# Optimization experiments

Measured on AMD Instinct MI355X. Metric: run time of the kernel, lower is better.

The kernel has to match this reference:

```python
import jax, jax.numpy as jnp
import numpy as np

B, S, D, H, L, V, FFM = 4, 2048, 512, 8, 6, 8000, 4
HD = D // H
FF = FFM * D


def setup_inputs() -> dict:
    key = jax.random.key(0)
    ks = jax.random.split(key, 12)
    sc = 0.02
    return {
        "tokens": jax.random.randint(ks[0], (B, S), 0, V),
        "embed": jax.random.normal(ks[1], (V, D), jnp.float32) * sc,
        "wq": jax.random.normal(ks[2], (L, D, D), jnp.float32) * sc,
        "wk": jax.random.normal(ks[3], (L, D, D), jnp.float32) * sc,
        "wv": jax.random.normal(ks[4], (L, D, D), jnp.float32) * sc,
        "wo": jax.random.normal(ks[5], (L, D, D), jnp.float32) * sc,
        "bo": jnp.zeros((L, D), jnp.float32),
        "w1": jax.random.normal(ks[6], (L, D, FF), jnp.float32) * sc,
        "b1": jnp.zeros((L, FF), jnp.float32),
        "w2": jax.random.normal(ks[7], (L, FF, D), jnp.float32) * sc,
        "b2": jnp.zeros((L, D), jnp.float32),
        "ln_g": jnp.ones((L, D), jnp.float32),
        "ln_b": jnp.zeros((L, D), jnp.float32),
        "lnf_g": jnp.ones((D,), jnp.float32),
        "lnf_b": jnp.zeros((D,), jnp.float32),
        "w_out": jax.random.normal(ks[8], (D, V), jnp.float32) * sc,
        "b_out": jnp.zeros((V,), jnp.float32),
    }


def _layernorm(x, g, b, eps=1e-5):
    m = jnp.mean(x, -1, keepdims=True)
    v = jnp.var(x, -1, keepdims=True)
    return (x - m) * jax.lax.rsqrt(v + eps) * g + b


def _pos_encoding():
    pos = jnp.arange(S, dtype=jnp.float32)[:, None]
    div = jnp.exp(jnp.arange(0, D, 2, dtype=jnp.float32) * (-np.log(10000.0) / D))
    pe = jnp.zeros((S, D), jnp.float32)
    pe = pe.at[:, 0::2].set(jnp.sin(pos * div))
    pe = pe.at[:, 1::2].set(jnp.cos(pos * div))
    return pe


def _forward(tokens, embed, wq, wk, wv, wo, bo, w1, b1, w2, b2, ln_g, ln_b,
             lnf_g, lnf_b, w_out, b_out):
    x = embed[tokens] + _pos_encoding()[None]  # [B,S,D]
    causal = jnp.tril(jnp.ones((S, S), bool))
    neg_inf = jnp.float32(-jnp.inf)
    # NOTE: original scales scores by 1/sqrt(n_embd) (key.weight.size(-1) == D)
    inv_scale = 1.0 / jnp.sqrt(jnp.float32(D))

    def block(x, p):
        pwq, pwk, pwv, pwo, pbo, pw1, pb1, pw2, pb2, g, b = p
        # attention sublayer (same LayerNorm params used for both sublayers,
        # matching the repo's reuse of add_and_norm_1)
        h = _layernorm(x, g, b)
        q = (h @ pwq).reshape(B, S, H, HD)
        k = (h @ pwk).reshape(B, S, H, HD)
        v = (h @ pwv).reshape(B, S, H, HD)
        scores = jnp.einsum('bqhd,bkhd->bhqk', q, k) * inv_scale
        scores = jnp.where(causal, scores, neg_inf)
        att = jax.nn.softmax(scores, axis=-1)
        o = jnp.einsum('bhqk,bkhd->bqhd', att, v).reshape(B, S, D)
        x = x + o @ pwo + pbo
        # FFN sublayer
        h2 = _layernorm(x, g, b)
        x = x + jax.nn.relu(h2 @ pw1 + pb1) @ pw2 + pb2
        return x, None

    params = (wq, wk, wv, wo, bo, w1, b1, w2, b2, ln_g, ln_b)
    x, _ = jax.lax.scan(block, x, params)
    x = _layernorm(x, lnf_g, lnf_b)
    logits = x @ w_out + b_out  # [B,S,V]
    return logits


def reference(tokens, embed, wq, wk, wv, wo, bo, w1, b1, w2, b2, ln_g, ln_b,
              lnf_g, lnf_b, w_out, b_out):
    return _forward(tokens, embed, wq, wk, wv, wo, bo, w1, b1, w2, b2,
                    ln_g, ln_b, lnf_g, lnf_b, w_out, b_out)
```

## Files before the change

### kernel.cpp

```cpp
#include <hip/hip_runtime.h>

#define Bsz 4
#define Ssz 2048
#define Dsz 512
#define Hsz 8
#define Lsz 6
#define Vsz 8000
#define FFsz 2048
#define Msz (Bsz*Ssz)
#define VszPad 8192

typedef unsigned short u16;
typedef unsigned int u32;
typedef __attribute__((ext_vector_type(8))) short bf16x8;
typedef __attribute__((ext_vector_type(4))) float f32x4;
typedef __attribute__((ext_vector_type(16))) float f32x16;
typedef __attribute__((ext_vector_type(4))) u32 u32x4;

__device__ __forceinline__ u16 f2b(float f) {
    union { float f; unsigned u; } x; x.f = f;
    return (u16)((x.u + 0x7fffu + ((x.u >> 16) & 1u)) >> 16);
}
__device__ __forceinline__ float b2f(u16 v) {
    union { u32 u; float f; } x; x.u = ((u32)v) << 16; return x.f;
}

#define GLOAD_LDS16(g, l) __builtin_amdgcn_global_load_lds( \
    (const __attribute__((address_space(1))) u32*)(g), \
    (__attribute__((address_space(3))) u32*)(l), 16, 0, 0)

__global__ __launch_bounds__(256) void embed_kernel(const int* __restrict__ tokens,
                                                    const float* __restrict__ embed,
                                                    u16* __restrict__ x) {
    int idx = blockIdx.x * 256 + threadIdx.x;
    int row = idx >> 8, p = idx & 255;
    int tok = tokens[row];
    int s = row & (Ssz - 1);
    float div = __expf((float)p * (-9.210340371976184f / 256.f));
    float ang = (float)s * div;
    float2 e = ((const float2*)(embed + (size_t)tok * Dsz))[p];
    u32 o = (u32)f2b(e.x + sinf(ang)) | ((u32)f2b(e.y + cosf(ang)) << 16);
    ((u32*)(x + (size_t)row * Dsz))[p] = o;
}

__global__ __launch_bounds__(256) void ln_kernel(const u16* __restrict__ x,
                                                 const float* __restrict__ g,
                                                 const float* __restrict__ bta,
                                                 u16* __restrict__ out) {
    int wave = threadIdx.x >> 6, lane = threadIdx.x & 63;
    int row = blockIdx.x * 4 + wave;
    bf16x8 a = ((const bf16x8*)(x + (size_t)row * Dsz))[lane];
    float vals[8];
    #pragma unroll
    for (int i = 0; i < 8; ++i) vals[i] = b2f((u16)a[i]);
    float s = 0.f;
    #pragma unroll
    for (int i = 0; i < 8; ++i) s += vals[i];
    #pragma unroll
    for (int o = 32; o; o >>= 1) s += __shfl_xor(s, o);
    float mean = s * (1.f / 512.f);
    float sq = 0.f;
    #pragma unroll
    for (int i = 0; i < 8; ++i) { float d = vals[i] - mean; sq += d * d; }
    #pragma unroll
    for (int o = 32; o; o >>= 1) sq += __shfl_xor(sq, o);
    float rstd = rsqrtf(sq * (1.f / 512.f) + 1e-5f);
    int base = lane * 8;
    bf16x8 rv;
    #pragma unroll
    for (int i = 0; i < 8; ++i)
        rv[i] = (short)f2b((vals[i] - mean) * rstd * g[base + i] + bta[base + i]);
    *(bf16x8*)(out + (size_t)row * Dsz + base) = rv;
}

__global__ __launch_bounds__(256) void tconv_kernel(const float* __restrict__ src,
                                                    u16* __restrict__ dst,
                                                    int R, int C,
                                                    size_t sstride, size_t dstride) {
    __shared__ float tile[32][33];
    const float* s = src + blockIdx.z * sstride;
    u16* d = dst + blockIdx.z * dstride;
    int c0 = blockIdx.x * 32, r0 = blockIdx.y * 32;
    int tx = threadIdx.x & 31, ty = threadIdx.x >> 5;
    #pragma unroll
    for (int i = 0; i < 32; i += 8)
        tile[ty + i][tx] = s[(size_t)(r0 + ty + i) * C + c0 + tx];
    __syncthreads();
    #pragma unroll
    for (int i = 0; i < 32; i += 8)
        d[(size_t)(c0 + ty + i) * R + r0 + tx] = f2b(tile[tx][ty + i]);
}

__global__ __launch_bounds__(256) void vtrans_kernel(const u16* __restrict__ qkv,
                                                     u16* __restrict__ vT) {
    __shared__ u16 tile[32][33];
    int bh = blockIdx.z, b = bh >> 3, hh = bh & 7;
    int s0 = blockIdx.x * 32, d0 = blockIdx.y * 32;
    int tx = threadIdx.x & 31, ty = threadIdx.x >> 5;
    #pragma unroll
    for (int i = 0; i < 32; i += 8)
        tile[ty + i][tx] = qkv[(size_t)(b * Ssz + s0 + ty + i) * 1536 + 1024 + hh * 64 + d0 + tx];
    __syncthreads();
    #pragma unroll
    for (int i = 0; i < 32; i += 8)
        vT[((size_t)bh * 64 + d0 + ty + i) * Ssz + s0 + tx] = tile[tx][ty + i];
}

template<bool BIAS, bool RES, bool RELU, bool OF32, bool OBF16, bool XN>
__global__ __launch_bounds__(256, 4) void gemm_kernel(const u16* __restrict__ A,
                                                   const u16* __restrict__ BT,
                                                   const float* __restrict__ bias,
                                                   const u16* __restrict__ res,
                                                   float* __restrict__ outf,
                                                   u16* __restrict__ outb,
                                                   int M, int N, int K) {
    __shared__ u16 As[128 * 64];
    __shared__ u16 Bs[128 * 64];
    int tid = threadIdx.x;
    int wave = tid >> 6, lane = tid & 63;
    int wm = wave >> 1, wn = wave & 1;
    int gx = gridDim.x;
    int bid = blockIdx.y * gx + blockIdx.x;
    int xcd = bid & 7, j = bid >> 3;
    int mblk, nblk;
    if (XN) { mblk = j >> 3; nblk = xcd * 8 + (j & 7); }
    else    { mblk = xcd * 8 + j / gx; nblk = j % gx; }
    int m0 = mblk * 128, n0 = nblk * 128;
    int lr = lane & 15, lg = lane >> 4;
    int srow = lane >> 3;
    int scol = (lane & 7) * 8;
    f32x4 acc[4][4] = {};
    for (int k0 = 0; k0 < K; k0 += 64) {
        #pragma unroll
        for (int i = 0; i < 4; ++i) {
            int chunk = wave * 4 + i;
            int r = chunk * 8 + srow;
            GLOAD_LDS16(A + (size_t)(m0 + r) * K + k0 + scol, &As[chunk * 512]);
            GLOAD_LDS16(BT + (size_t)(n0 + r) * K + k0 + scol, &Bs[chunk * 512]);
        }
        __syncthreads();
        #pragma unroll
        for (int kk = 0; kk < 2; ++kk) {
            bf16x8 af[4], bfr[4];
            #pragma unroll
            for (int m = 0; m < 4; ++m)
                af[m] = *(const bf16x8*)(As + (wm * 64 + m * 16 + lr) * 64 + kk * 32 + lg * 8);
            #pragma unroll
            for (int n = 0; n < 4; ++n)
                bfr[n] = *(const bf16x8*)(Bs + (wn * 64 + n * 16 + lr) * 64 + kk * 32 + lg * 8);
            #pragma unroll
            for (int m = 0; m < 4; ++m)
                #pragma unroll
                for (int n = 0; n < 4; ++n)
                    acc[m][n] = __builtin_amdgcn_mfma_f32_16x16x32_bf16(af[m], bfr[n], acc[m][n], 0, 0, 0);
        }
        __syncthreads();
    }
    #pragma unroll
    for (int m = 0; m < 4; ++m) {
        int row = m0 + wm * 64 + m * 16 + lg * 4;
        #pragma unroll
        for (int n = 0; n < 4; ++n) {
            int col = n0 + wn * 64 + n * 16 + lr;
            if (col < N) {
                float bv = BIAS ? bias[col] : 0.f;
                #pragma unroll
                for (int j2 = 0; j2 < 4; ++j2) {
                    float v = acc[m][n][j2] + bv;
                    if (RES) v += b2f(res[(size_t)(row + j2) * N + col]);
                    if (RELU) v = fmaxf(v, 0.f);
                    if (OF32) outf[(size_t)(row + j2) * N + col] = v;
                    if (OBF16) outb[(size_t)(row + j2) * N + col] = f2b(v);
                }
            }
        }
    }
}

__global__ __launch_bounds__(256, 2) void flash4_kernel(const u16* __restrict__ qkv,
                                                        const u16* __restrict__ vT,
                                                        u16* __restrict__ o) {
    __shared__ u16 Ks[64 * 64];
    __shared__ u16 Vs[64 * 64];
    int blk = blockIdx.x;
    int bh = blk & 31;
    int c = 15 - (blk >> 5);
    int b = bh >> 3, hh = bh & 7;
    int tid = threadIdx.x, wave = tid >> 6, lane = tid & 63;
    int l31 = lane & 31, h5 = lane >> 5;
    int g = c * 4 + wave;
    int qg = g * 32 + l31;
    int ext = (g >> 1) + 1;
    int nt = 2 * c + 2;
    const float cs = 0.044194173824159216f;

    bf16x8 qf[4];
    {
        const u16* qrow = qkv + (size_t)(b * Ssz + qg) * 1536 + hh * 64;
        #pragma unroll
        for (int cb = 0; cb < 4; ++cb)
            qf[cb] = *(const bf16x8*)(qrow + cb * 16 + h5 * 8);
    }
    f32x16 Oa0 = {}, Oa1 = {};
    float m_run = -1e30f, l_run = 0.f;
    int sr = tid >> 3;
    int sc2 = (tid & 7) * 8;
    const u16* kbase = qkv + (size_t)(b * Ssz) * 1536 + 512 + hh * 64;
    const u16* vbase = vT + (size_t)bh * 64 * Ssz;

    for (int kt = 0; kt < nt; ++kt) {
        #pragma unroll
        for (int p = 0; p < 2; ++p) {
            int r = p * 32 + sr;
            bf16x8 kv_ = *(const bf16x8*)(kbase + (size_t)(kt * 64 + r) * 1536 + sc2);
            bf16x8 vv  = *(const bf16x8*)(vbase + (size_t)r * Ssz + kt * 64 + sc2);
            int byte = (r * 128 + sc2 * 2) ^ ((r & 7) << 4);
            *(bf16x8*)((char*)Ks + byte) = kv_;
            *(bf16x8*)((char*)Vs + byte) = vv;
        }
        __syncthreads();
        if (kt < ext) {
            bool dtile = (kt == ext - 1);
            int mts = (dtile && !(g & 1)) ? 1 : 2;
            f32x16 st[2] = {};
            __builtin_amdgcn_s_setprio(1);
            #pragma unroll
            for (int mt = 0; mt < 2; ++mt)
                if (mt < mts) {
                    int r = mt * 32 + l31;
                    #pragma unroll
                    for (int cb = 0; cb < 4; ++cb) {
                        int byte = (r * 128 + (cb * 16 + h5 * 8) * 2) ^ ((r & 7) << 4);
                        bf16x8 kf = *(const bf16x8*)((char*)Ks + byte);
                        st[mt] = __builtin_amdgcn_mfma_f32_32x32x16_bf16(kf, qf[cb], st[mt], 0, 0, 0);
                    }
                }
            __builtin_amdgcn_s_setprio(0);
            float pmax = -1e30f;
            #pragma unroll
            for (int mt = 0; mt < 2; ++mt)
                if (mt < mts)
                    #pragma unroll
                    for (int r = 0; r < 16; ++r) {
                        float v = st[mt][r];
                        if (dtile) {
                            int kglob = kt * 64 + mt * 32 + (r & 3) + 8 * (r >> 2) + 4 * h5;
                            if (kglob > qg) v = -1e30f;
                        }
                        st[mt][r] = v;
                        pmax = fmaxf(pmax, v);
                    }
            pmax = fmaxf(pmax, __shfl_xor(pmax, 32));
            if (!__all(pmax - m_run <= 181.019336f)) {
                float mn = fmaxf(m_run, pmax);
                float al = __expf((m_run - mn) * cs);
                l_run *= al;
                #pragma unroll
                for (int r = 0; r < 16; ++r) {
                    int qloc = (r & 3) + 8 * (r >> 2) + 4 * h5;
                    float alr = __shfl(al, qloc);
                    Oa0[r] *= alr; Oa1[r] *= alr;
                }
                m_run = mn;
            }
            float ls = 0.f;
            u32 pk[2][8];
            #pragma unroll
            for (int mt = 0; mt < 2; ++mt)
                if (mt < mts)
                    #pragma unroll
                    for (int w = 0; w < 8; ++w) {
                        float p0 = __expf((st[mt][2 * w]     - m_run) * cs);
                        float p1 = __expf((st[mt][2 * w + 1] - m_run) * cs);
                        ls += p0 + p1;
                        pk[mt][w] = (u32)f2b(p0) | ((u32)f2b(p1) << 16);
                    }
            l_run += ls + __shfl_xor(ls, 32);
            __builtin_amdgcn_s_setprio(1);
            #pragma unroll
            for (int mt = 0; mt < 2; ++mt)
                if (mt < mts) {
                    u32 pko[8];
                    #pragma unroll
                    for (int w = 0; w < 8; ++w)
                        pko[w] = __shfl_xor(pk[mt][w], 32);
                    #pragma unroll
                    for (int kbl = 0; kbl < 2; ++kbl) {
                        int kb = mt * 2 + kbl;
                        u32x4 aw;
                        #pragma unroll
                        for (int w = 0; w < 4; ++w) {
                            int widx = 4 * kbl + 2 * h5 + (w & 1);
                            bool own = (w < 2) != (h5 == 1);
                            aw[w] = own ? pk[mt][widx] : pko[widx];
                        }
                        bf16x8 af = __builtin_bit_cast(bf16x8, aw);
                        #pragma unroll
                        for (int dt = 0; dt < 2; ++dt) {
                            int r = dt * 32 + l31;
                            int byte = (r * 128 + (kb * 16 + h5 * 8) * 2) ^ ((r & 7) << 4);
                            bf16x8 vf = *(const bf16x8*)((char*)Vs + byte);
                            if (dt == 0) Oa0 = __builtin_amdgcn_mfma_f32_32x32x16_bf16(af, vf, Oa0, 0, 0, 0);
                            else         Oa1 = __builtin_amdgcn_mfma_f32_32x32x16_bf16(af, vf, Oa1, 0, 0, 0);
                        }
                    }
                }
            __builtin_amdgcn_s_setprio(0);
        }
        __syncthreads();
    }
    float rln = 1.f / l_run;
    u16* obase = o + (size_t)(b * Ssz) * Dsz + hh * 64;
    #pragma unroll
    for (int r = 0; r < 16; ++r) {
        int qloc = (r & 3) + 8 * (r >> 2) + 4 * h5;
        float s = __shfl(rln, qloc);
        u16* orow = obase + (size_t)(g * 32 + qloc) * Dsz + l31;
        orow[0]  = f2b(Oa0[r] * s);
        orow[32] = f2b(Oa1[r] * s);
    }
}

extern "C" void kernel_launch(void* const* d_in, const int* in_sizes, int n_in,
                              void* d_out, int out_size, void* d_ws, size_t ws_size,
                              hipStream_t stream) {
    (void)in_sizes; (void)n_in; (void)out_size; (void)ws_size;
    const int*   tokens = (const int*)d_in[0];
    const float* embed  = (const float*)d_in[1];
    const float* wq     = (const float*)d_in[2];
    const float* wk     = (const float*)d_in[3];
    const float* wv     = (const float*)d_in[4];
    const float* wo     = (const float*)d_in[5];
    const float* bo     = (const float*)d_in[6];
    const float* w1     = (const float*)d_in[7];
    const float* b1     = (const float*)d_in[8];
    const float* w2     = (const float*)d_in[9];
    const float* b2     = (const float*)d_in[10];
    const float* ln_g   = (const float*)d_in[11];
    const float* ln_b   = (const float*)d_in[12];
    const float* lnf_g  = (const float*)d_in[13];
    const float* lnf_b  = (const float*)d_in[14];
    const float* w_out  = (const float*)d_in[15];
    const float* b_out  = (const float*)d_in[16];
    float* out = (float*)d_out;

    char* ws = (char*)d_ws;
    size_t off = 0;
    auto alloc = [&](size_t bytes) {
        void* p = ws + off;
        off += (bytes + 255) & ~(size_t)255;
        return p;
    };
    u16*   x     = (u16*)alloc((size_t)Msz * Dsz * 2);
    u16*   h     = (u16*)alloc((size_t)Msz * Dsz * 2);
    u16*   qkv   = (u16*)alloc((size_t)Msz * 1536 * 2);
    u16*   vT    = (u16*)alloc((size_t)Bsz * Hsz * 64 * Ssz * 2);
    u16*   ob    = (u16*)alloc((size_t)Msz * Dsz * 2);
    u16*   ffh   = (u16*)alloc((size_t)Msz * FFsz * 2);
    u16*   wqkvT = (u16*)alloc((size_t)Lsz * 3 * Dsz * Dsz * 2);
    u16*   woT   = (u16*)alloc((size_t)Lsz * Dsz * Dsz * 2);
    u16*   w1T   = (u16*)alloc((size_t)Lsz * FFsz * Dsz * 2);
    u16*   w2T   = (u16*)alloc((size_t)Lsz * Dsz * FFsz * 2);
    u16*   w_outT= (u16*)alloc((size_t)VszPad * Dsz * 2);

    dim3 tb(256);
    size_t dd = (size_t)Dsz * Dsz;
    hipMemsetAsync(w_outT + (size_t)Vsz * Dsz, 0, (size_t)(VszPad - Vsz) * Dsz * 2, stream);
    tconv_kernel<<<dim3(16, 16, Lsz), tb, 0, stream>>>(wq, wqkvT + 0 * dd, Dsz, Dsz, dd, 3 * dd);
    tconv_kernel<<<dim3(16, 16, Lsz), tb, 0, stream>>>(wk, wqkvT + 1 * dd, Dsz, Dsz, dd, 3 * dd);
    tconv_kernel<<<dim3(16, 16, Lsz), tb, 0, stream>>>(wv, wqkvT + 2 * dd, Dsz, Dsz, dd, 3 * dd);
    tconv_kernel<<<dim3(16, 16, Lsz), tb, 0, stream>>>(wo, woT, Dsz, Dsz, dd, dd);
    tconv_kernel<<<dim3(64, 16, Lsz), tb, 0, stream>>>(w1, w1T, Dsz, FFsz, (size_t)Dsz * FFsz, (size_t)FFsz * Dsz);
    tconv_kernel<<<dim3(16, 64, Lsz), tb, 0, stream>>>(w2, w2T, FFsz, Dsz, (size_t)FFsz * Dsz, (size_t)Dsz * FFsz);
    tconv_kernel<<<dim3(250, 16, 1), tb, 0, stream>>>(w_out, w_outT, Dsz, Vsz, 0, 0);

    embed_kernel<<<Msz * 256 / 256, tb, 0, stream>>>(tokens, embed, x);

    for (int l = 0; l < Lsz; ++l) {
        ln_kernel<<<Msz / 4, tb, 0, stream>>>(x, ln_g + l * Dsz, ln_b + l * Dsz, h);
        gemm_kernel<false, false, false, false, true, false><<<dim3(12, Msz / 128), tb, 0, stream>>>(
            h, wqkvT + (size_t)l * 3 * dd, nullptr, nullptr, nullptr, qkv, Msz, 1536, Dsz);
        vtrans_kernel<<<dim3(Ssz / 32, 2, Bsz * Hsz), tb, 0, stream>>>(qkv, vT);
        flash4_kernel<<<dim3(512), tb, 0, stream>>>(qkv, vT, ob);
        gemm_kernel<true, true, false, false, true, false><<<dim3(4, Msz / 128), tb, 0, stream>>>(
            ob, woT + (size_t)l * dd, bo + l * Dsz, x, nullptr, x, Msz, Dsz, Dsz);
        ln_kernel<<<Msz / 4, tb, 0, stream>>>(x, ln_g + l * Dsz, ln_b + l * Dsz, h);
        gemm_kernel<true, false, true, false, true, false><<<dim3(16, Msz / 128), tb, 0, stream>>>(
            h, w1T + (size_t)l * FFsz * Dsz, b1 + l * FFsz, nullptr, nullptr, ffh, Msz, FFsz, Dsz);
        gemm_kernel<true, true, false, false, true, false><<<dim3(4, Msz / 128), tb, 0, stream>>>(
            ffh, w2T + (size_t)l * Dsz * FFsz, b2 + l * Dsz, x, nullptr, x, Msz, Dsz, FFsz);
    }
    ln_kernel<<<Msz / 4, tb, 0, stream>>>(x, lnf_g, lnf_b, h);
    gemm_kernel<true, false, false, true, false, true><<<dim3(64, Msz / 128), tb, 0, stream>>>(
        h, w_outT, b_out, nullptr, out, nullptr, Msz, Vsz, Dsz);
}
```

Baseline: 1.659 ms.

## Double-buffer K/V tiles in flash attention and halve M-tile for narrow GEMMs

The attention kernel now keeps two LDS buffers for K and V. It issues the global loads for the next tile into registers before computing on the current one, then writes them to the other buffer after the compute, so each iteration needs one barrier instead of two and the load latency is hidden. The GEMM kernel gets a template M-tile factor, and the N=512 projection and FFN-down GEMMs use 64-row tiles. This doubles their block count (from 256 blocks) to fill more CUs, at the cost of more B-tile reloads and extra LDS and register pressure in attention.

```diff
diff --git a/kernel.cpp b/kernel.cpp
--- a/kernel.cpp
+++ b/kernel.cpp
@@ -106,7 +106,7 @@
         vT[((size_t)bh * 64 + d0 + ty + i) * Ssz + s0 + tx] = tile[tx][ty + i];
 }
 
-template<bool BIAS, bool RES, bool RELU, bool OF32, bool OBF16, bool XN>
+template<bool BIAS, bool RES, bool RELU, bool OF32, bool OBF16, bool XN, int BMF>
 __global__ __launch_bounds__(256, 4) void gemm_kernel(const u16* __restrict__ A,
                                                    const u16* __restrict__ BT,
                                                    const float* __restrict__ bias,
@@ -114,7 +114,7 @@
                                                    float* __restrict__ outf,
                                                    u16* __restrict__ outb,
                                                    int M, int N, int K) {
-    __shared__ u16 As[128 * 64];
+    __shared__ u16 As[BMF * 32 * 64];
     __shared__ u16 Bs[128 * 64];
     int tid = threadIdx.x;
     int wave = tid >> 6, lane = tid & 63;
@@ -124,32 +124,37 @@
     int xcd = bid & 7, j = bid >> 3;
     int mblk, nblk;
     if (XN) { mblk = j >> 3; nblk = xcd * 8 + (j & 7); }
-    else    { mblk = xcd * 8 + j / gx; nblk = j % gx; }
-    int m0 = mblk * 128, n0 = nblk * 128;
+    else    { int sm = gridDim.y >> 3; mblk = xcd * sm + j / gx; nblk = j % gx; }
+    int m0 = mblk * (BMF * 32), n0 = nblk * 128;
     int lr = lane & 15, lg = lane >> 4;
     int srow = lane >> 3;
     int scol = (lane & 7) * 8;
-    f32x4 acc[4][4] = {};
+    f32x4 acc[BMF][4] = {};
     for (int k0 = 0; k0 < K; k0 += 64) {
+        #pragma unroll
+        for (int i = 0; i < BMF; ++i) {
+            int chunk = wave * BMF + i;
+            int r = chunk * 8 + srow;
+            GLOAD_LDS16(A + (size_t)(m0 + r) * K + k0 + scol, &As[chunk * 512]);
+        }
         #pragma unroll
         for (int i = 0; i < 4; ++i) {
             int chunk = wave * 4 + i;
             int r = chunk * 8 + srow;
-            GLOAD_LDS16(A + (size_t)(m0 + r) * K + k0 + scol, &As[chunk * 512]);
             GLOAD_LDS16(BT + (size_t)(n0 + r) * K + k0 + scol, &Bs[chunk * 512]);
         }
         __syncthreads();
         #pragma unroll
         for (int kk = 0; kk < 2; ++kk) {
-            bf16x8 af[4], bfr[4];
-            #pragma unroll
-            for (int m = 0; m < 4; ++m)
-                af[m] = *(const bf16x8*)(As + (wm * 64 + m * 16 + lr) * 64 + kk * 32 + lg * 8);
+            bf16x8 af[BMF], bfr[4];
+            #pragma unroll
+            for (int m = 0; m < BMF; ++m)
+                af[m] = *(const bf16x8*)(As + (wm * (BMF * 16) + m * 16 + lr) * 64 + kk * 32 + lg * 8);
             #pragma unroll
             for (int n = 0; n < 4; ++n)
                 bfr[n] = *(const bf16x8*)(Bs + (wn * 64 + n * 16 + lr) * 64 + kk * 32 + lg * 8);
             #pragma unroll
-            for (int m = 0; m < 4; ++m)
+            for (int m = 0; m < BMF; ++m)
                 #pragma unroll
                 for (int n = 0; n < 4; ++n)
                     acc[m][n] = __builtin_amdgcn_mfma_f32_16x16x32_bf16(af[m], bfr[n], acc[m][n], 0, 0, 0);
@@ -157,8 +162,8 @@
         __syncthreads();
     }
     #pragma unroll
-    for (int m = 0; m < 4; ++m) {
-        int row = m0 + wm * 64 + m * 16 + lg * 4;
+    for (int m = 0; m < BMF; ++m) {
+        int row = m0 + wm * (BMF * 16) + m * 16 + lg * 4;
         #pragma unroll
         for (int n = 0; n < 4; ++n) {
             int col = n0 + wn * 64 + n * 16 + lr;
@@ -177,11 +182,11 @@
     }
 }
 
-__global__ __launch_bounds__(256, 2) void flash4_kernel(const u16* __restrict__ qkv,
+__global__ __launch_bounds__(256, 2) void flash5_kernel(const u16* __restrict__ qkv,
                                                         const u16* __restrict__ vT,
                                                         u16* __restrict__ o) {
-    __shared__ u16 Ks[64 * 64];
-    __shared__ u16 Vs[64 * 64];
+    __shared__ u16 Ks[2][64 * 64];
+    __shared__ u16 Vs[2][64 * 64];
     int blk = blockIdx.x;
     int bh = blk & 31;
     int c = 15 - (blk >> 5);
@@ -207,18 +212,33 @@
     int sc2 = (tid & 7) * 8;
     const u16* kbase = qkv + (size_t)(b * Ssz) * 1536 + 512 + hh * 64;
     const u16* vbase = vT + (size_t)bh * 64 * Ssz;
+    int byteA = (sr * 128 + sc2 * 2) ^ ((sr & 7) << 4);
+    int byteB = ((sr + 32) * 128 + sc2 * 2) ^ ((sr & 7) << 4);
+
+    {
+        bf16x8 kA = *(const bf16x8*)(kbase + (size_t)sr * 1536 + sc2);
+        bf16x8 kB = *(const bf16x8*)(kbase + (size_t)(32 + sr) * 1536 + sc2);
+        bf16x8 vA = *(const bf16x8*)(vbase + (size_t)sr * Ssz + sc2);
+        bf16x8 vB = *(const bf16x8*)(vbase + (size_t)(32 + sr) * Ssz + sc2);
+        *(bf16x8*)((char*)Ks[0] + byteA) = kA;
+        *(bf16x8*)((char*)Ks[0] + byteB) = kB;
+        *(bf16x8*)((char*)Vs[0] + byteA) = vA;
+        *(bf16x8*)((char*)Vs[0] + byteB) = vB;
+    }
+    __syncthreads();
 
     for (int kt = 0; kt < nt; ++kt) {
-        #pragma unroll
-        for (int p = 0; p < 2; ++p) {
-            int r = p * 32 + sr;
-            bf16x8 kv_ = *(const bf16x8*)(kbase + (size_t)(kt * 64 + r) * 1536 + sc2);
-            bf16x8 vv  = *(const bf16x8*)(vbase + (size_t)r * Ssz + kt * 64 + sc2);
-            int byte = (r * 128 + sc2 * 2) ^ ((r & 7) << 4);
-            *(bf16x8*)((char*)Ks + byte) = kv_;
-            *(bf16x8*)((char*)Vs + byte) = vv;
-        }
-        __syncthreads();
+        int cur = kt & 1;
+        bool pf = (kt + 1 < nt);
+        bf16x8 kA, kB, vA, vB;
+        if (pf) {
+            kA = *(const bf16x8*)(kbase + (size_t)((kt + 1) * 64 + sr) * 1536 + sc2);
+            kB = *(const bf16x8*)(kbase + (size_t)((kt + 1) * 64 + 32 + sr) * 1536 + sc2);
+            vA = *(const bf16x8*)(vbase + (size_t)sr * Ssz + (kt + 1) * 64 + sc2);
+            vB = *(const bf16x8*)(vbase + (size_t)(32 + sr) * Ssz + (kt + 1) * 64 + sc2);
+        }
+        const u16* Kc = Ks[cur];
+        const u16* Vc = Vs[cur];
         if (kt < ext) {
             bool dtile = (kt == ext - 1);
             int mts = (dtile && !(g & 1)) ? 1 : 2;
@@ -231,7 +251,7 @@
                     #pragma unroll
                     for (int cb = 0; cb < 4; ++cb) {
                         int byte = (r * 128 + (cb * 16 + h5 * 8) * 2) ^ ((r & 7) << 4);
-                        bf16x8 kf = *(const bf16x8*)((char*)Ks + byte);
+                        bf16x8 kf = *(const bf16x8*)((char*)Kc + byte);
                         st[mt] = __builtin_amdgcn_mfma_f32_32x32x16_bf16(kf, qf[cb], st[mt], 0, 0, 0);
                     }
                 }
@@ -299,13 +319,21 @@
                         for (int dt = 0; dt < 2; ++dt) {
                             int r = dt * 32 + l31;
                             int byte = (r * 128 + (kb * 16 + h5 * 8) * 2) ^ ((r & 7) << 4);
-                            bf16x8 vf = *(const bf16x8*)((char*)Vs + byte);
+                            bf16x8 vf = *(const bf16x8*)((char*)Vc + byte);
                             if (dt == 0) Oa0 = __builtin_amdgcn_mfma_f32_32x32x16_bf16(af, vf, Oa0, 0, 0, 0);
                             else         Oa1 = __builtin_amdgcn_mfma_f32_32x32x16_bf16(af, vf, Oa1, 0, 0, 0);
                         }
                     }
                 }
             __builtin_amdgcn_s_setprio(0);
+        }
+        if (pf) {
+            u16* Kn = Ks[cur ^ 1];
+            u16* Vn = Vs[cur ^ 1];
+            *(bf16x8*)((char*)Kn + byteA) = kA;
+            *(bf16x8*)((char*)Kn + byteB) = kB;
+            *(bf16x8*)((char*)Vn + byteA) = vA;
+            *(bf16x8*)((char*)Vn + byteB) = vB;
         }
         __syncthreads();
     }
@@ -378,19 +406,19 @@
 
     for (int l = 0; l < Lsz; ++l) {
         ln_kernel<<<Msz / 4, tb, 0, stream>>>(x, ln_g + l * Dsz, ln_b + l * Dsz, h);
-        gemm_kernel<false, false, false, false, true, false><<<dim3(12, Msz / 128), tb, 0, stream>>>(
+        gemm_kernel<false, false, false, false, true, false, 4><<<dim3(12, Msz / 128), tb, 0, stream>>>(
             h, wqkvT + (size_t)l * 3 * dd, nullptr, nullptr, nullptr, qkv, Msz, 1536, Dsz);
         vtrans_kernel<<<dim3(Ssz / 32, 2, Bsz * Hsz), tb, 0, stream>>>(qkv, vT);
-        flash4_kernel<<<dim3(512), tb, 0, stream>>>(qkv, vT, ob);
-        gemm_kernel<true, true, false, false, true, false><<<dim3(4, Msz / 128), tb, 0, stream>>>(
+        flash5_kernel<<<dim3(512), tb, 0, stream>>>(qkv, vT, ob);
+        gemm_kernel<true, true, false, false, true, false, 2><<<dim3(4, Msz / 64), tb, 0, stream>>>(
             ob, woT + (size_t)l * dd, bo + l * Dsz, x, nullptr, x, Msz, Dsz, Dsz);
         ln_kernel<<<Msz / 4, tb, 0, stream>>>(x, ln_g + l * Dsz, ln_b + l * Dsz, h);
-        gemm_kernel<true, false, true, false, true, false><<<dim3(16, Msz / 128), tb, 0, stream>>>(
+        gemm_kernel<true, false, true, false, true, false, 4><<<dim3(16, Msz / 128), tb, 0, stream>>>(
             h, w1T + (size_t)l * FFsz * Dsz, b1 + l * FFsz, nullptr, nullptr, ffh, Msz, FFsz, Dsz);
-        gemm_kernel<true, true, false, false, true, false><<<dim3(4, Msz / 128), tb, 0, stream>>>(
+        gemm_kernel<true, true, false, false, true, false, 2><<<dim3(4, Msz / 64), tb, 0, stream>>>(
             ffh, w2T + (size_t)l * Dsz * FFsz, b2 + l * Dsz, x, nullptr, x, Msz, Dsz, FFsz);
     }
     ln_kernel<<<Msz / 4, tb, 0, stream>>>(x, lnf_g, lnf_b, h);
-    gemm_kernel<true, false, false, true, false, true><<<dim3(64, Msz / 128), tb, 0, stream>>>(
+    gemm_kernel<true, false, false, true, false, true, 4><<<dim3(64, Msz / 128), tb, 0, stream>>>(
         h, w_outT, b_out, nullptr, out, nullptr, Msz, Vsz, Dsz);
 }
```

Result: faster. 1.569 ms (-5.4%).
